# Performance work log

Hardware: AMD Instinct MI355X
Metric: run time of the kernel (lower is better)

Reference implementation:

```python
import jax, jax.numpy as jnp
import numpy as np

NUM_CLASSES = 2
IGNORE_INDEX = 0
B, H, W = 4, 512, 512
BIG_I = 2 ** 30  # int sentinel for 'no seed yet'
INF = jnp.float32(1e9)  # distance when a column/image has no seed


def _edt_to_seed(seed):
    """Exact 2D Euclidean distance transform: distance from every pixel to the
    nearest True pixel in `seed` [H, W] (matches scipy distance_transform_edt
    applied to an image whose zeros are `seed`).
    Pass 1: 1D nearest-seed distance down each column via cummax/cummin scans.
    Pass 2: exact lower envelope across rows by brute-force min over k:
            D^2(i,j) = min_k ( (j-k)^2 + g(i,k)^2 ).
    """
    h, w = seed.shape
    rows = jnp.arange(h, dtype=jnp.int32)[:, None]              # [H,1]
    last = jax.lax.cummax(jnp.where(seed, rows, -1), axis=0)     # last seed above
    d_fwd = jnp.where(last >= 0, rows - last, BIG_I)
    nxt = jax.lax.cummin(jnp.where(seed, rows, BIG_I), axis=0, reverse=True)
    d_bwd = jnp.where(nxt < BIG_I, nxt - rows, BIG_I)
    g = jnp.minimum(d_fwd, d_bwd)                                # [H,W] int
    g2 = jnp.where(g >= BIG_I // 2, INF * INF, (g * g).astype(jnp.float32))
    cols = jnp.arange(w, dtype=jnp.float32)
    sq = (cols[:, None] - cols[None, :]) ** 2                    # [Wj,Wk]
    d2 = jnp.min(g2[:, None, :] + sq[None, :, :], axis=-1)       # [H,Wj]
    return jnp.sqrt(d2)


def _distance_map_one(tgt):
    """tgt: [H, W] int labels -> [num_classes, H, W] signed distance maps."""
    maps = []
    for c in range(NUM_CLASSES):
        if c == IGNORE_INDEX:
            maps.append(jnp.zeros(tgt.shape, jnp.float32))
            continue
        mask = tgt == c
        pos_dist = _edt_to_seed(~mask)   # edt(posmask): dist to nearest background
        neg_dist = _edt_to_seed(mask)    # edt(negmask): dist to nearest foreground
        present = jnp.any(mask)          # 'if mask.sum() > 0' guard
        maps.append(jnp.where(present, neg_dist - pos_dist, 0.0))
    return jnp.stack(maps, axis=0)


def setup_inputs() -> dict:
    key = jax.random.key(0)
    k1, k2 = jax.random.split(key)
    pred = jax.random.normal(k1, (B, NUM_CLASSES, H, W), dtype=jnp.float32)
    target = jax.random.randint(k2, (B, H, W), 0, 2, dtype=jnp.int32)
    return {"pred": pred, "target": target}


def reference(pred, target):
    p = jax.nn.softmax(pred, axis=1)                         # [B,C,H,W]
    # sequential over batch to bound the [H,W,W] EDT intermediate
    dmaps = jax.lax.map(_distance_map_one, target)           # [B,C,H,W]
    return jnp.mean(p * dmaps)
```

## Files before the change

kernel.cpp:

```cpp
#include <hip/hip_runtime.h>
#include <math.h>

#define BB 4
#define HH 512
#define WW 512
#define HWSZ (HH * WW)

#define NPAIR 8
#define TCH   32
#define CROWS 16
#define COLS_BLOCKS 128
#define ROWS_BLOCKS (BB * HH)
#define BIGR 0x100000

#define SK(x) ((x) + ((x) >> 5))


__global__ __launch_bounds__(256) void edt_cols_kernel(
    const int* __restrict__ target,
    unsigned int* __restrict__ gpack,
    int* __restrict__ flags)
{
    int blk = blockIdx.x;
    int b = blk >> 5;
    int tile = blk & 31;
    int tid = threadIdx.x;
    int p = tid & (NPAIR - 1);
    int ch = tid >> 3;
    int j = tile * 16 + 2 * p;
    int r0 = ch * CROWS;

    const int2* t2 = (const int2*)(target + b * HWSZ + j);

    unsigned int m0 = 0, m1 = 0;
#pragma unroll
    for (int i = 0; i < CROWS; ++i) {
        int2 v = t2[(r0 + i) * (WW / 2)];
        m0 |= (unsigned int)(v.x == 1) << i;
        m1 |= (unsigned int)(v.y == 1) << i;
    }
    unsigned int q0 = m0 ^ 0xFFFFu, q1 = m1 ^ 0xFFFFu;

    __shared__ int sLN[TCH][17], sFN[TCH][17];
    __shared__ int sLP[TCH][17], sFP[TCH][17];
    __shared__ int sBN[TCH][17], sAN[TCH][17];
    __shared__ int sBP[TCH][17], sAP[TCH][17];
    __shared__ int sCnt;

    int c0 = 2 * p, c1 = 2 * p + 1;
    sLN[ch][c0] = m0 ? (r0 + 31 - __builtin_clz(m0)) : -1;
    sFN[ch][c0] = m0 ? (r0 + __builtin_ctz(m0))      : BIGR;
    sLP[ch][c0] = q0 ? (r0 + 31 - __builtin_clz(q0)) : -1;
    sFP[ch][c0] = q0 ? (r0 + __builtin_ctz(q0))      : BIGR;
    sLN[ch][c1] = m1 ? (r0 + 31 - __builtin_clz(m1)) : -1;
    sFN[ch][c1] = m1 ? (r0 + __builtin_ctz(m1))      : BIGR;
    sLP[ch][c1] = q1 ? (r0 + 31 - __builtin_clz(q1)) : -1;
    sFP[ch][c1] = q1 ? (r0 + __builtin_ctz(q1))      : BIGR;

    int cnt = __popc(m0) + __popc(m1);
#pragma unroll
    for (int off = 32; off > 0; off >>= 1) cnt += __shfl_down(cnt, off, 64);
    if (tid == 0) sCnt = 0;
    __syncthreads();
    if ((tid & 63) == 0) atomicAdd(&sCnt, cnt);

    if (tid < 16) {
        int befN = -1, befP = -1;
        for (int k = 0; k < TCH; ++k) {
            sBN[k][tid] = befN; sBP[k][tid] = befP;
            int ln = sLN[k][tid], lp = sLP[k][tid];
            if (ln >= 0) befN = ln;
            if (lp >= 0) befP = lp;
        }
        int aftN = BIGR, aftP = BIGR;
        for (int k = TCH - 1; k >= 0; --k) {
            sAN[k][tid] = aftN; sAP[k][tid] = aftP;
            int fn = sFN[k][tid], fp = sFP[k][tid];
            if (fn < BIGR) aftN = fn;
            if (fp < BIGR) aftP = fp;
        }
    }
    __syncthreads();

    int bN0 = sBN[ch][c0], bP0 = sBP[ch][c0], aN0 = sAN[ch][c0], aP0 = sAP[ch][c0];
    int bN1 = sBN[ch][c1], bP1 = sBP[ch][c1], aN1 = sAN[ch][c1], aP1 = sAP[ch][c1];
    uint2* gp2 = (uint2*)(gpack + b * HWSZ + j);

#pragma unroll
    for (int i = 0; i < CROWS; ++i) {
        int row = r0 + i;
        uint2 outv;
        {
            unsigned int below = m0 << (31 - i), above = m0 >> i;
            unsigned int df = below ? (unsigned int)__builtin_clz(below)
                                    : (bN0 >= 0 ? (unsigned int)(row - bN0) : 0xFFFFu);
            unsigned int db = above ? (unsigned int)__builtin_ctz(above)
                                    : (aN0 < BIGR ? (unsigned int)(aN0 - row) : 0xFFFFu);
            unsigned int gN = df < db ? df : db; if (gN > 0xFFFFu) gN = 0xFFFFu;
            below = q0 << (31 - i); above = q0 >> i;
            df = below ? (unsigned int)__builtin_clz(below)
                       : (bP0 >= 0 ? (unsigned int)(row - bP0) : 0xFFFFu);
            db = above ? (unsigned int)__builtin_ctz(above)
                       : (aP0 < BIGR ? (unsigned int)(aP0 - row) : 0xFFFFu);
            unsigned int gP = df < db ? df : db; if (gP > 0xFFFFu) gP = 0xFFFFu;
            outv.x = gN | (gP << 16);
        }
        {
            unsigned int below = m1 << (31 - i), above = m1 >> i;
            unsigned int df = below ? (unsigned int)__builtin_clz(below)
                                    : (bN1 >= 0 ? (unsigned int)(row - bN1) : 0xFFFFu);
            unsigned int db = above ? (unsigned int)__builtin_ctz(above)
                                    : (aN1 < BIGR ? (unsigned int)(aN1 - row) : 0xFFFFu);
            unsigned int gN = df < db ? df : db; if (gN > 0xFFFFu) gN = 0xFFFFu;
            below = q1 << (31 - i); above = q1 >> i;
            df = below ? (unsigned int)__builtin_clz(below)
                       : (bP1 >= 0 ? (unsigned int)(row - bP1) : 0xFFFFu);
            db = above ? (unsigned int)__builtin_ctz(above)
                       : (aP1 < BIGR ? (unsigned int)(aP1 - row) : 0xFFFFu);
            unsigned int gP = df < db ? df : db; if (gP > 0xFFFFu) gP = 0xFFFFu;
            outv.y = gN | (gP << 16);
        }
        gp2[row * (WW / 2)] = outv;
    }

    if (tid == 0) flags[blk] = (sCnt > 0);
}

__global__ __launch_bounds__(64) void edt_rows_kernel(
    const unsigned int* __restrict__ gpack,
    const float* __restrict__ pred,
    float* __restrict__ partials)
{
    __shared__ float g2n[SK(511) + 1];
    __shared__ float g2p[SK(511) + 1];

    int bi = blockIdx.x;
    int b = bi >> 9;
    int i = bi & (HH - 1);
    int k = threadIdx.x;
    int j0 = 8 * k;

    const float* p0 = pred + (b * 2 + 0) * HWSZ + i * WW + j0;
    const float* p1 = pred + (b * 2 + 1) * HWSZ + i * WW + j0;
    float4 a0 = *(const float4*)(p0);
    float4 a1 = *(const float4*)(p0 + 4);
    float4 c0 = *(const float4*)(p1);
    float4 c1 = *(const float4*)(p1 + 4);

    const uint4* gp4 = (const uint4*)(gpack + b * HWSZ + i * WW);
    uint4 ga = gp4[k];
    uint4 gb = gp4[k + 64];

    unsigned int va[4] = {ga.x, ga.y, ga.z, ga.w};
    unsigned int vb[4] = {gb.x, gb.y, gb.z, gb.w};
#pragma unroll
    for (int t = 0; t < 4; ++t) {
        int idx = 4 * k + t;
        unsigned int gN = va[t] & 0xFFFFu, gP = va[t] >> 16;
        g2n[SK(idx)] = (gN == 0xFFFFu) ? 1e18f : (float)(gN * gN);
        g2p[SK(idx)] = (gP == 0xFFFFu) ? 1e18f : (float)(gP * gP);
        int idx2 = 256 + 4 * k + t;
        gN = vb[t] & 0xFFFFu; gP = vb[t] >> 16;
        g2n[SK(idx2)] = (gN == 0xFFFFu) ? 1e18f : (float)(gN * gN);
        g2p[SK(idx2)] = (gP == 0xFFFFu) ? 1e18f : (float)(gP * gP);
    }
    __syncthreads();

    const float* sel[8];
    float bs[8], sgn[8];
#pragma unroll
    for (int jj = 0; jj < 8; ++jj) {
        float on = g2n[SK(j0 + jj)];
        float op = g2p[SK(j0 + jj)];
        bool fg = (on == 0.0f);
        sel[jj] = fg ? g2p : g2n;
        bs[jj]  = fg ? op : on;
        sgn[jj] = fg ? -1.0f : 1.0f;
    }
    for (int r = 1; r < WW; ++r) {
        float sq = (float)(r * r);
        float mx = 0.0f;
#pragma unroll
        for (int jj = 0; jj < 8; ++jj) mx = fmaxf(mx, bs[jj]);
        if (sq >= mx) break;
#pragma unroll
        for (int jj = 0; jj < 8; ++jj) {
            int kl = j0 + jj - r; kl = kl < 0 ? 0 : kl;
            int kr = j0 + jj + r; kr = kr > (WW - 1) ? (WW - 1) : kr;
            bs[jj] = fminf(bs[jj], sq + sel[jj][SK(kl)]);
            bs[jj] = fminf(bs[jj], sq + sel[jj][SK(kr)]);
        }
    }

    float x0[8] = {a0.x, a0.y, a0.z, a0.w, a1.x, a1.y, a1.z, a1.w};
    float x1[8] = {c0.x, c0.y, c0.z, c0.w, c1.x, c1.y, c1.z, c1.w};
    float acc = 0.0f;
#pragma unroll
    for (int jj = 0; jj < 8; ++jj) {
        float dist = sgn[jj] * sqrtf(bs[jj]);
        float prob = 1.0f / (1.0f + __expf(x0[jj] - x1[jj]));
        acc += prob * dist;
    }
#pragma unroll
    for (int off = 32; off > 0; off >>= 1) acc += __shfl_down(acc, off, 64);
    if (k == 0) partials[bi] = acc;
}

__global__ __launch_bounds__(64) void finalize_kernel(
    const int* __restrict__ flags,
    const float* __restrict__ partials,
    float* __restrict__ out)
{
    int k = threadIdx.x;

    double presd[BB];
#pragma unroll
    for (int b = 0; b < BB; ++b) {
        int f = (k < 32) ? flags[b * 32 + k] : 0;
        presd[b] = (__ballot(f != 0) != 0ULL) ? 1.0 : 0.0;
    }

    const float4* p4 = (const float4*)partials;
    double s = 0.0;
#pragma unroll
    for (int t = 0; t < 8; ++t) {
        int v4 = k + 64 * t;
        float4 v = p4[v4];
        double g = presd[v4 >> 7];
        s += g * ((double)v.x + (double)v.y + (double)v.z + (double)v.w);
    }
#pragma unroll
    for (int off = 32; off > 0; off >>= 1) s += __shfl_down(s, off, 64);
    if (k == 0)
        out[0] = (float)(s * (1.0 / 2097152.0));
}

extern "C" void kernel_launch(void* const* d_in, const int* in_sizes, int n_in,
                              void* d_out, int out_size, void* d_ws, size_t ws_size,
                              hipStream_t stream) {
    const float* pred = (const float*)d_in[0];
    const int* target = (const int*)d_in[1];
    float* out = (float*)d_out;

    char* ws = (char*)d_ws;
    int* flags = (int*)(ws + 0);
    float* partials = (float*)(ws + 1024);
    unsigned int* gpack = (unsigned int*)(ws + 32768);

    edt_cols_kernel<<<COLS_BLOCKS, 256, 0, stream>>>(target, gpack, flags);
    edt_rows_kernel<<<ROWS_BLOCKS, 64, 0, stream>>>(gpack, pred, partials);
    finalize_kernel<<<1, 64, 0, stream>>>(flags, partials, out);
}
```

Before: 73.32 us.

## Pack target into column bit-words and compute column distances inside rows kernel

```diff
diff --git a/kernel.cpp b/kernel.cpp
--- a/kernel.cpp
+++ b/kernel.cpp
@@ -5,175 +5,130 @@
 #define HH 512
 #define WW 512
 #define HWSZ (HH * WW)
-
-#define NPAIR 8
-#define TCH   32
-#define CROWS 16
-#define COLS_BLOCKS 128
-#define ROWS_BLOCKS (BB * HH)
-#define BIGR 0x100000
+#define ROWS_BLOCKS 256
 
 #define SK(x) ((x) + ((x) >> 5))
 
 
-__global__ __launch_bounds__(256) void edt_cols_kernel(
+__global__ __launch_bounds__(256) void pack_kernel(
     const int* __restrict__ target,
-    unsigned int* __restrict__ gpack,
+    unsigned int* __restrict__ cw,
     int* __restrict__ flags)
 {
-    int blk = blockIdx.x;
-    int b = blk >> 5;
-    int tile = blk & 31;
-    int tid = threadIdx.x;
-    int p = tid & (NPAIR - 1);
-    int ch = tid >> 3;
-    int j = tile * 16 + 2 * p;
-    int r0 = ch * CROWS;
-
-    const int2* t2 = (const int2*)(target + b * HWSZ + j);
-
-    unsigned int m0 = 0, m1 = 0;
-#pragma unroll
-    for (int i = 0; i < CROWS; ++i) {
-        int2 v = t2[(r0 + i) * (WW / 2)];
-        m0 |= (unsigned int)(v.x == 1) << i;
-        m1 |= (unsigned int)(v.y == 1) << i;
-    }
-    unsigned int q0 = m0 ^ 0xFFFFu, q1 = m1 ^ 0xFFFFu;
-
-    __shared__ int sLN[TCH][17], sFN[TCH][17];
-    __shared__ int sLP[TCH][17], sFP[TCH][17];
-    __shared__ int sBN[TCH][17], sAN[TCH][17];
-    __shared__ int sBP[TCH][17], sAP[TCH][17];
     __shared__ int sCnt;
-
-    int c0 = 2 * p, c1 = 2 * p + 1;
-    sLN[ch][c0] = m0 ? (r0 + 31 - __builtin_clz(m0)) : -1;
-    sFN[ch][c0] = m0 ? (r0 + __builtin_ctz(m0))      : BIGR;
-    sLP[ch][c0] = q0 ? (r0 + 31 - __builtin_clz(q0)) : -1;
-    sFP[ch][c0] = q0 ? (r0 + __builtin_ctz(q0))      : BIGR;
-    sLN[ch][c1] = m1 ? (r0 + 31 - __builtin_clz(m1)) : -1;
-    sFN[ch][c1] = m1 ? (r0 + __builtin_ctz(m1))      : BIGR;
-    sLP[ch][c1] = q1 ? (r0 + 31 - __builtin_clz(q1)) : -1;
-    sFP[ch][c1] = q1 ? (r0 + __builtin_ctz(q1))      : BIGR;
-
-    int cnt = __popc(m0) + __popc(m1);
+    int gid = blockIdx.x * 256 + threadIdx.x;
+    int b = gid >> 13;
+    int rem = gid & 8191;
+    int w = rem >> 9;
+    int col = rem & 511;
+
+    const int* t = target + b * HWSZ + (w << 5) * WW + col;
+    unsigned int word = 0;
+#pragma unroll
+    for (int i = 0; i < 32; ++i)
+        word |= (unsigned int)(t[i * WW] == 1) << i;
+    cw[gid] = word;
+
+    int cnt = __popc(word);
 #pragma unroll
     for (int off = 32; off > 0; off >>= 1) cnt += __shfl_down(cnt, off, 64);
-    if (tid == 0) sCnt = 0;
+    if (threadIdx.x == 0) sCnt = 0;
     __syncthreads();
-    if ((tid & 63) == 0) atomicAdd(&sCnt, cnt);
-
-    if (tid < 16) {
-        int befN = -1, befP = -1;
-        for (int k = 0; k < TCH; ++k) {
-            sBN[k][tid] = befN; sBP[k][tid] = befP;
-            int ln = sLN[k][tid], lp = sLP[k][tid];
-            if (ln >= 0) befN = ln;
-            if (lp >= 0) befP = lp;
-        }
-        int aftN = BIGR, aftP = BIGR;
-        for (int k = TCH - 1; k >= 0; --k) {
-            sAN[k][tid] = aftN; sAP[k][tid] = aftP;
-            int fn = sFN[k][tid], fp = sFP[k][tid];
-            if (fn < BIGR) aftN = fn;
-            if (fp < BIGR) aftP = fp;
-        }
-    }
+    if ((threadIdx.x & 63) == 0) atomicAdd(&sCnt, cnt);
     __syncthreads();
-
-    int bN0 = sBN[ch][c0], bP0 = sBP[ch][c0], aN0 = sAN[ch][c0], aP0 = sAP[ch][c0];
-    int bN1 = sBN[ch][c1], bP1 = sBP[ch][c1], aN1 = sAN[ch][c1], aP1 = sAP[ch][c1];
-    uint2* gp2 = (uint2*)(gpack + b * HWSZ + j);
-
-#pragma unroll
-    for (int i = 0; i < CROWS; ++i) {
-        int row = r0 + i;
-        uint2 outv;
-        {
-            unsigned int below = m0 << (31 - i), above = m0 >> i;
-            unsigned int df = below ? (unsigned int)__builtin_clz(below)
-                                    : (bN0 >= 0 ? (unsigned int)(row - bN0) : 0xFFFFu);
-            unsigned int db = above ? (unsigned int)__builtin_ctz(above)
-                                    : (aN0 < BIGR ? (unsigned int)(aN0 - row) : 0xFFFFu);
-            unsigned int gN = df < db ? df : db; if (gN > 0xFFFFu) gN = 0xFFFFu;
-            below = q0 << (31 - i); above = q0 >> i;
-            df = below ? (unsigned int)__builtin_clz(below)
-                       : (bP0 >= 0 ? (unsigned int)(row - bP0) : 0xFFFFu);
-            db = above ? (unsigned int)__builtin_ctz(above)
-                       : (aP0 < BIGR ? (unsigned int)(aP0 - row) : 0xFFFFu);
-            unsigned int gP = df < db ? df : db; if (gP > 0xFFFFu) gP = 0xFFFFu;
-            outv.x = gN | (gP << 16);
-        }
-        {
-            unsigned int below = m1 << (31 - i), above = m1 >> i;
-            unsigned int df = below ? (unsigned int)__builtin_clz(below)
-                                    : (bN1 >= 0 ? (unsigned int)(row - bN1) : 0xFFFFu);
-            unsigned int db = above ? (unsigned int)__builtin_ctz(above)
-                                    : (aN1 < BIGR ? (unsigned int)(aN1 - row) : 0xFFFFu);
-            unsigned int gN = df < db ? df : db; if (gN > 0xFFFFu) gN = 0xFFFFu;
-            below = q1 << (31 - i); above = q1 >> i;
-            df = below ? (unsigned int)__builtin_clz(below)
-                       : (bP1 >= 0 ? (unsigned int)(row - bP1) : 0xFFFFu);
-            db = above ? (unsigned int)__builtin_ctz(above)
-                       : (aP1 < BIGR ? (unsigned int)(aP1 - row) : 0xFFFFu);
-            unsigned int gP = df < db ? df : db; if (gP > 0xFFFFu) gP = 0xFFFFu;
-            outv.y = gN | (gP << 16);
-        }
-        gp2[row * (WW / 2)] = outv;
-    }
-
-    if (tid == 0) flags[blk] = (sCnt > 0);
-}
-
-__global__ __launch_bounds__(64) void edt_rows_kernel(
-    const unsigned int* __restrict__ gpack,
+    if (threadIdx.x == 0) flags[blockIdx.x] = (sCnt > 0);
+}
+
+__global__ __launch_bounds__(512) void rows_kernel(
+    const unsigned int* __restrict__ cw,
     const float* __restrict__ pred,
     float* __restrict__ partials)
 {
-    __shared__ float g2n[SK(511) + 1];
-    __shared__ float g2p[SK(511) + 1];
-
-    int bi = blockIdx.x;
-    int b = bi >> 9;
-    int i = bi & (HH - 1);
-    int k = threadIdx.x;
-    int j0 = 8 * k;
-
-    const float* p0 = pred + (b * 2 + 0) * HWSZ + i * WW + j0;
-    const float* p1 = pred + (b * 2 + 1) * HWSZ + i * WW + j0;
+    __shared__ unsigned int sW[16 * 512];
+    __shared__ float g2n[8][SK(511) + 1], g2p[8][SK(511) + 1];
+
+    int blk = blockIdx.x;
+    int b = blk >> 6;
+    int g = blk & 63;
+    int tid = threadIdx.x;
+    int w = tid >> 6, lane = tid & 63;
+    int row = 8 * g + w;
+    int j0 = 8 * lane;
+
+    const float* p0 = pred + (b * 2 + 0) * HWSZ + row * WW + j0;
+    const float* p1 = pred + (b * 2 + 1) * HWSZ + row * WW + j0;
     float4 a0 = *(const float4*)(p0);
     float4 a1 = *(const float4*)(p0 + 4);
     float4 c0 = *(const float4*)(p1);
     float4 c1 = *(const float4*)(p1 + 4);
 
-    const uint4* gp4 = (const uint4*)(gpack + b * HWSZ + i * WW);
-    uint4 ga = gp4[k];
-    uint4 gb = gp4[k + 64];
-
-    unsigned int va[4] = {ga.x, ga.y, ga.z, ga.w};
-    unsigned int vb[4] = {gb.x, gb.y, gb.z, gb.w};
-#pragma unroll
-    for (int t = 0; t < 4; ++t) {
-        int idx = 4 * k + t;
-        unsigned int gN = va[t] & 0xFFFFu, gP = va[t] >> 16;
-        g2n[SK(idx)] = (gN == 0xFFFFu) ? 1e18f : (float)(gN * gN);
-        g2p[SK(idx)] = (gP == 0xFFFFu) ? 1e18f : (float)(gP * gP);
-        int idx2 = 256 + 4 * k + t;
-        gN = vb[t] & 0xFFFFu; gP = vb[t] >> 16;
-        g2n[SK(idx2)] = (gN == 0xFFFFu) ? 1e18f : (float)(gN * gN);
-        g2p[SK(idx2)] = (gP == 0xFFFFu) ? 1e18f : (float)(gP * gP);
-    }
+    const unsigned int* cwb = cw + b * 8192;
+#pragma unroll
+    for (int t = 0; t < 16; ++t)
+        sW[tid + 512 * t] = cwb[tid + 512 * t];
     __syncthreads();
+
+    int wr = row >> 5, bit = row & 31;
+    float* G2N = g2n[w];
+    float* G2P = g2p[w];
+    unsigned int loMask = 0xFFFFFFFFu >> (31 - bit);
+    unsigned int hiMask = 0xFFFFFFFFu << bit;
+#pragma unroll
+    for (int t = 0; t < 8; ++t) {
+        int col = lane + (t << 6);
+        unsigned int Wr = sW[(wr << 9) + col];
+        int dUp, dDn;
+        unsigned int m = Wr & loMask;
+        if (m) dUp = bit - (31 - __builtin_clz(m));
+        else {
+            dUp = 0x7FFFFFFF;
+            for (int q = wr - 1; q >= 0; --q) {
+                unsigned int W = sW[(q << 9) + col];
+                if (W) { dUp = row - ((q << 5) + 31 - __builtin_clz(W)); break; }
+            }
+        }
+        m = Wr & hiMask;
+        if (m) dDn = __builtin_ctz(m) - bit;
+        else {
+            dDn = 0x7FFFFFFF;
+            for (int q = wr + 1; q < 16; ++q) {
+                unsigned int W = sW[(q << 9) + col];
+                if (W) { dDn = (q << 5) + __builtin_ctz(W) - row; break; }
+            }
+        }
+        int gN = min(dUp, dDn);
+        G2N[SK(col)] = (gN > 511) ? 1e18f : (float)(gN * gN);
+        unsigned int Vr = ~Wr;
+        m = Vr & loMask;
+        if (m) dUp = bit - (31 - __builtin_clz(m));
+        else {
+            dUp = 0x7FFFFFFF;
+            for (int q = wr - 1; q >= 0; --q) {
+                unsigned int W = ~sW[(q << 9) + col];
+                if (W) { dUp = row - ((q << 5) + 31 - __builtin_clz(W)); break; }
+            }
+        }
+        m = Vr & hiMask;
+        if (m) dDn = __builtin_ctz(m) - bit;
+        else {
+            dDn = 0x7FFFFFFF;
+            for (int q = wr + 1; q < 16; ++q) {
+                unsigned int W = ~sW[(q << 9) + col];
+                if (W) { dDn = (q << 5) + __builtin_ctz(W) - row; break; }
+            }
+        }
+        int gP = min(dUp, dDn);
+        G2P[SK(col)] = (gP > 511) ? 1e18f : (float)(gP * gP);
+    }
 
     const float* sel[8];
     float bs[8], sgn[8];
 #pragma unroll
     for (int jj = 0; jj < 8; ++jj) {
-        float on = g2n[SK(j0 + jj)];
-        float op = g2p[SK(j0 + jj)];
+        float on = G2N[SK(j0 + jj)];
+        float op = G2P[SK(j0 + jj)];
         bool fg = (on == 0.0f);
-        sel[jj] = fg ? g2p : g2n;
+        sel[jj] = fg ? G2P : G2N;
         bs[jj]  = fg ? op : on;
         sgn[jj] = fg ? -1.0f : 1.0f;
     }
@@ -203,7 +158,7 @@
     }
 #pragma unroll
     for (int off = 32; off > 0; off >>= 1) acc += __shfl_down(acc, off, 64);
-    if (k == 0) partials[bi] = acc;
+    if (lane == 0) partials[b * HH + row] = acc;
 }
 
 __global__ __launch_bounds__(64) void finalize_kernel(
@@ -226,8 +181,8 @@
     for (int t = 0; t < 8; ++t) {
         int v4 = k + 64 * t;
         float4 v = p4[v4];
-        double g = presd[v4 >> 7];
-        s += g * ((double)v.x + (double)v.y + (double)v.z + (double)v.w);
+        double gd = presd[v4 >> 7];
+        s += gd * ((double)v.x + (double)v.y + (double)v.z + (double)v.w);
     }
 #pragma unroll
     for (int off = 32; off > 0; off >>= 1) s += __shfl_down(s, off, 64);
@@ -245,9 +200,9 @@
     char* ws = (char*)d_ws;
     int* flags = (int*)(ws + 0);
     float* partials = (float*)(ws + 1024);
-    unsigned int* gpack = (unsigned int*)(ws + 32768);
-
-    edt_cols_kernel<<<COLS_BLOCKS, 256, 0, stream>>>(target, gpack, flags);
-    edt_rows_kernel<<<ROWS_BLOCKS, 64, 0, stream>>>(gpack, pred, partials);
+    unsigned int* cw = (unsigned int*)(ws + 32768);
+
+    pack_kernel<<<128, 256, 0, stream>>>(target, cw, flags);
+    rows_kernel<<<ROWS_BLOCKS, 512, 0, stream>>>(cw, pred, partials);
     finalize_kernel<<<1, 64, 0, stream>>>(flags, partials, out);
 }
```

Result: no change. 72.96 us (-0.5%).
